# Optimization experiments

Hardware: AMD Instinct MI355X
Metric: run time of the kernel (lower is better)

Reference implementation:

```python
import jax, jax.numpy as jnp
import numpy as np

B, N_TOK, D = 32, 1024, 1024
CH, PS, NP = 3, 16, 32  # channels, patch_size, n_patches (sample_size // patch_size)
EPS = 1e-5


def setup_inputs() -> dict:
    key = jax.random.key(0)
    k1, k2 = jax.random.split(key)
    x = jax.random.normal(k1, (B, N_TOK, D), dtype=jnp.float32)
    ln_w = jnp.ones((D,), dtype=jnp.float32)
    ln_b = jnp.zeros((D,), dtype=jnp.float32)
    W = jax.random.normal(k2, (CH * PS * PS, D), dtype=jnp.float32) * (1.0 / np.sqrt(D))
    b = jnp.zeros((CH * PS * PS,), dtype=jnp.float32)
    return {"x": x, "ln_w": ln_w, "ln_b": ln_b, "W": W, "b": b}


def reference(x, ln_w, ln_b, W, b):
    # LayerNorm over last dim
    mean = jnp.mean(x, axis=-1, keepdims=True)
    var = jnp.mean(jnp.square(x - mean), axis=-1, keepdims=True)
    h = (x - mean) * jax.lax.rsqrt(var + EPS) * ln_w + ln_b
    # SiLU
    h = h * jax.nn.sigmoid(h)
    # Linear: [B, N, D] @ [D, ph*pw*c] + bias
    y = jnp.einsum('bnd,od->bno', h, W) + b  # [B, N_TOK, PS*PS*CH]
    # rearrange 'b (h w) (ph pw c) -> b c (h ph) (w pw)'
    y = y.reshape(B, NP, NP, PS, PS, CH)           # b h w ph pw c
    y = y.transpose(0, 5, 1, 3, 2, 4)              # b c h ph w pw
    y = y.reshape(B, CH, NP * PS, NP * PS)
    return y
```

## Files before the change

kernel.cpp:

```cpp
#include <hip/hip_runtime.h>
#include <hip/hip_bf16.h>

#define M_TOT 32768
#define DDIM  1024
#define ODIM  768
#define LN_EPS 1e-5f

typedef __attribute__((__ext_vector_type__(8))) short bf16x8;
typedef __attribute__((__ext_vector_type__(4))) float f32x4;

__device__ __forceinline__ unsigned short f2bf(float f) {
  union { __hip_bfloat16 h; unsigned short u; } cv;
  cv.h = __float2bfloat16(f);
  return cv.u;
}

__device__ __forceinline__ float silu_f(float v) {
  return v / (1.f + __expf(-v));
}

__global__ void wconv_kernel(const float4* __restrict__ Wf, ushort4* __restrict__ Wb, int n4) {
  int i = blockIdx.x * blockDim.x + threadIdx.x;
  if (i >= n4) return;
  float4 v = Wf[i];
  ushort4 o;
  o.x = f2bf(v.x); o.y = f2bf(v.y); o.z = f2bf(v.z); o.w = f2bf(v.w);
  Wb[i] = o;
}

__global__ __launch_bounds__(256)
void ln_silu_kernel(const float* __restrict__ x, const float* __restrict__ lnw,
                    const float* __restrict__ lnb, __hip_bfloat16* __restrict__ h)
{
  const int tid  = threadIdx.x;
  const int lane = tid & 63;
  const int wid  = tid >> 6;
  const int row  = blockIdx.x * 4 + wid;

  const float4* xr = (const float4*)(x + (size_t)row * DDIM);
  float4 v[4];
#pragma unroll
  for (int jj = 0; jj < 4; ++jj) v[jj] = xr[lane + 64 * jj];

  float s = 0.f, ss = 0.f;
#pragma unroll
  for (int jj = 0; jj < 4; ++jj) {
    float4 a = v[jj];
    s  += a.x + a.y + a.z + a.w;
    ss += a.x * a.x + a.y * a.y + a.z * a.z + a.w * a.w;
  }
#pragma unroll
  for (int off = 1; off < 64; off <<= 1) {
    s  += __shfl_xor(s, off);
    ss += __shfl_xor(ss, off);
  }
  const float mean = s * (1.f / 1024.f);
  const float rstd = rsqrtf(ss * (1.f / 1024.f) - mean * mean + LN_EPS);

  ushort4* hr = (ushort4*)(h + (size_t)row * DDIM);
#pragma unroll
  for (int jj = 0; jj < 4; ++jj) {
    float4 wv = ((const float4*)lnw)[lane + 64 * jj];
    float4 bv = ((const float4*)lnb)[lane + 64 * jj];
    float4 a  = v[jj];
    float e0 = silu_f((a.x - mean) * rstd * wv.x + bv.x);
    float e1 = silu_f((a.y - mean) * rstd * wv.y + bv.y);
    float e2 = silu_f((a.z - mean) * rstd * wv.z + bv.z);
    float e3 = silu_f((a.w - mean) * rstd * wv.w + bv.w);
    ushort4 o; o.x = f2bf(e0); o.y = f2bf(e1); o.z = f2bf(e2); o.w = f2bf(e3);
    hr[lane + 64 * jj] = o;
  }
}

#define GBM 256
#define GBN 192
#define ABYTES 16384
#define BUFB   28672

__device__ __forceinline__ void gload16(const void* g, void* l) {
  __builtin_amdgcn_global_load_lds(
      (const __attribute__((address_space(1))) unsigned int*)g,
      (__attribute__((address_space(3))) unsigned int*)l, 16, 0, 0);
}

#define VMW(n) asm volatile("s_waitcnt vmcnt(" #n ")" ::: "memory")

__global__ __launch_bounds__(512, 2)
void gemm_kernel(const __hip_bfloat16* __restrict__ h,
                 const __hip_bfloat16* __restrict__ Wb,
                 const float* __restrict__ bias,
                 float* __restrict__ out)
{
  __shared__ char smem[4 * BUFB];
  const int tid  = threadIdx.x;
  const int lane = tid & 63;
  const int w    = tid >> 6;

  const int wg = blockIdx.x;
  const int sv = ((wg & 7) << 6) + (wg >> 3);
  const int mt = sv >> 2, nt = sv & 3;
  const int m0 = mt << 8, n0 = nt * GBN;

  const __hip_bfloat16* aP[2]; int aD[2];
#pragma unroll
  for (int q = 0; q < 2; ++q) {
    int s = (q << 9) + tid;
    int row = s >> 2, chk = s & 3;
    aP[q] = h + (size_t)(m0 + row) * DDIM + ((chk ^ ((row >> 1) & 3)) << 3);
    aD[q] = s << 4;
  }
  const bool roleB = (tid < 256);
  const __hip_bfloat16* bP0; int bD0;
  const __hip_bfloat16* bP1; int bD1;
  {
    int s = tid, row = s >> 2, chk = s & 3;
    bP0 = Wb + (size_t)(n0 + row) * DDIM + ((chk ^ ((row >> 1) & 3)) << 3);
    bD0 = ABYTES + (s << 4);
    int s2 = 512 + (tid & 255);
    int r2 = s2 >> 2, c2 = s2 & 3;
    bP1 = Wb + (size_t)(n0 + r2) * DDIM + ((c2 ^ ((r2 >> 1) & 3)) << 3);
    bD1 = ABYTES + (s2 << 4);
  }

  const int wm = w >> 1, wn = w & 1;
  const int lr = lane & 15, lq = lane >> 4;
  int aRd[4], bRd[6];
#pragma unroll
  for (int i = 0; i < 4; ++i) {
    int row = wm * 64 + i * 16 + lr;
    aRd[i] = row * 64 + ((lq ^ ((row >> 1) & 3)) << 4);
  }
#pragma unroll
  for (int j = 0; j < 6; ++j) {
    int row = wn * 96 + j * 16 + lr;
    bRd[j] = ABYTES + row * 64 + ((lq ^ ((row >> 1) & 3)) << 4);
  }

  auto stageA = [&](int t) {
    char* b = smem + (t & 3) * BUFB;
    const int k0 = t << 5;
    gload16(aP[0] + k0, b + aD[0]);
    gload16(aP[1] + k0, b + aD[1]);
  };
  auto stageB = [&](int t) {
    char* b = smem + (t & 3) * BUFB;
    const int k0 = t << 5;
    gload16(bP0 + k0, b + bD0);
    if (roleB) gload16(bP1 + k0, b + bD1);
  };

  f32x4 acc[4][6];
#pragma unroll
  for (int i = 0; i < 4; ++i)
#pragma unroll
    for (int j = 0; j < 6; ++j)
      acc[i][j] = (f32x4){0.f, 0.f, 0.f, 0.f};

  stageA(0); stageB(0);
  stageA(1); stageB(1);
  stageA(2); stageB(2);

  for (int t = 0; t < 32; ++t) {
    if (t <= 29)      { if (roleB) VMW(8); else VMW(6); }
    else if (t == 30) { if (roleB) VMW(4); else VMW(3); }
    else              { VMW(0); }
    __builtin_amdgcn_s_barrier();
    asm volatile("" ::: "memory");

    const char* bb = smem + (t & 3) * BUFB;
    bf16x8 af[4], bf0[3], bf1[3];
#pragma unroll
    for (int i = 0; i < 4; ++i) af[i]  = *(const bf16x8*)(bb + aRd[i]);
#pragma unroll
    for (int j = 0; j < 3; ++j) bf0[j] = *(const bf16x8*)(bb + bRd[j]);
    if (t < 29) stageA(t + 3);

    __builtin_amdgcn_s_setprio(1);
#pragma unroll
    for (int i = 0; i < 4; ++i)
#pragma unroll
      for (int j = 0; j < 3; ++j)
        acc[i][j] = __builtin_amdgcn_mfma_f32_16x16x32_bf16(af[i], bf0[j], acc[i][j], 0, 0, 0);
    __builtin_amdgcn_s_setprio(0);

#pragma unroll
    for (int j = 0; j < 3; ++j) bf1[j] = *(const bf16x8*)(bb + bRd[3 + j]);
    if (t < 29) stageB(t + 3);

    __builtin_amdgcn_s_setprio(1);
#pragma unroll
    for (int i = 0; i < 4; ++i)
#pragma unroll
      for (int j = 0; j < 3; ++j)
        acc[i][3 + j] = __builtin_amdgcn_mfma_f32_16x16x32_bf16(af[i], bf1[j], acc[i][3 + j], 0, 0, 0);
    __builtin_amdgcn_s_setprio(0);
  }

  const int b   = m0 >> 10;
  const int hl0 = (m0 & 1023) >> 5;
  float bv[6]; int cj[6], pwj[6], prj[6];
#pragma unroll
  for (int j = 0; j < 6; ++j) {
    int o = wn * 96 + j * 16 + lr;
    bv[j]  = bias[n0 + o];
    cj[j]  = o % 3;
    int oq = o / 3;
    pwj[j] = oq & 15;
    prj[j] = oq >> 4;
  }
  float* ldsF = (float*)smem;

#pragma unroll
  for (int g = 0; g < 16; ++g) {
    if (wm == (g >> 2)) {
      const int i_f = g & 3;
#pragma unroll
      for (int j = 0; j < 6; ++j)
#pragma unroll
        for (int r = 0; r < 4; ++r) {
          const int tk = lq * 4 + r;
          ldsF[((cj[j] * 4 + prj[j]) << 8) + (tk << 4) + (pwj[j] ^ (lq << 2))] =
              acc[i_f][j][r] + bv[j];
        }
    }
    __syncthreads();
    const int hh = hl0 + (g >> 1);
#pragma unroll
    for (int u = 0; u < 2; ++u) {
      if (u == 1 && tid >= 256) break;
      const int f   = (u << 9) + tid;
      const int c   = f >> 8;
      const int pr  = (f >> 6) & 3;
      const int tk  = (f >> 2) & 15;
      const int pw0 = (f & 3) << 2;
      const int lqw = tk >> 2;
      float4 v = *(const float4*)(ldsF + (((c * 4 + pr) << 8) + (tk << 4)
                                          + (pw0 ^ (lqw << 2))));
      const size_t idx = (((size_t)(b * 3 + c)) << 18)
                       + (size_t)((hh << 4) + (nt << 2) + pr) * 512
                       + ((g & 1) << 8) + (tk << 4) + pw0;
      *(float4*)(out + idx) = v;
    }
    __syncthreads();
  }
}

#define BM 64
#define BK 32
#define NTHR 1024
#define LDS_BYTES 53760

__global__ __launch_bounds__(NTHR, 4)
void fused_kernel(const float* __restrict__ x,
                  const float* __restrict__ lnw,
                  const float* __restrict__ lnb,
                  const float* __restrict__ Wf,
                  const float* __restrict__ bias,
                  float* __restrict__ out)
{
  extern __shared__ char smem[];
  char* AsBase = smem;
  char* BsBase = smem + 4096;
  float* smean = (float*)(smem + 53248);
  float* srstd = smean + BM;

  const int tid = threadIdx.x;
  const int m0  = blockIdx.x * BM;
  const int bb   = m0 >> 10;
  const int h0   = (m0 & 1023) >> 5;

  {
    const int row = tid >> 4;
    const int sub = tid & 15;
    const float4* xr = (const float4*)(x + (size_t)(m0 + row) * DDIM);
    float s = 0.f, ss = 0.f;
#pragma unroll 4
    for (int j = 0; j < 16; ++j) {
      float4 v = xr[sub + (j << 4)];
      s  += v.x + v.y + v.z + v.w;
      ss += v.x * v.x + v.y * v.y + v.z * v.z + v.w * v.w;
    }
#pragma unroll
    for (int off = 1; off < 16; off <<= 1) {
      s  += __shfl_xor(s, off);
      ss += __shfl_xor(ss, off);
    }
    if (sub == 0) {
      float mean = s * (1.f / 1024.f);
      float var  = ss * (1.f / 1024.f) - mean * mean;
      smean[row] = mean;
      srstd[row] = rsqrtf(var + LN_EPS);
    }
  }
  __syncthreads();

  const int arow  = tid >> 4;
  const int acol2 = tid & 15;
  const int aOff  = (m0 + arow) * DDIM + (acol2 << 1);
  const int aDst  = (arow << 6) + ((((acol2 >> 2) ^ ((arow >> 2) & 3)) << 4)) + ((acol2 & 3) << 2);
  const float aMean = smean[arow];
  const float aRstd = srstd[arow];

  int bOffF[6], bDstF[6];
#pragma unroll
  for (int c = 0; c < 6; ++c) {
    int idx = tid + (c << 10);
    int r = idx >> 3, c4 = idx & 7;
    bOffF[c] = r * DDIM + (c4 << 2);
    bDstF[c] = (r << 6) + ((((c4 >> 1) ^ ((r >> 2) & 3)) << 4)) + ((c4 & 1) << 3);
  }

  const int lane = tid & 63;
  const int wid  = tid >> 6;
  const int lr   = lane & 15;
  const int lq   = lane >> 4;
  const int kswz = (lq ^ ((lr >> 2) & 3)) << 4;
  int aRd[4], bRd[3];
#pragma unroll
  for (int i = 0; i < 4; ++i) aRd[i] = (((i << 4) + lr) << 6) + kswz;
#pragma unroll
  for (int j = 0; j < 3; ++j) bRd[j] = ((wid * 48 + (j << 4) + lr) << 6) + kswz;

  float2 aReg, lwReg, lbReg;
  float4 bRegF[6];

  auto loadTile = [&](int tt) {
    const int k0 = tt * BK;
    aReg  = *(const float2*)(x + aOff + k0);
    lwReg = *(const float2*)(lnw + (acol2 << 1) + k0);
    lbReg = *(const float2*)(lnb + (acol2 << 1) + k0);
#pragma unroll
    for (int c = 0; c < 6; ++c)
      bRegF[c] = *(const float4*)(Wf + bOffF[c] + k0);
  };

  auto storeTile = [&]() {
    float hx = (aReg.x - aMean) * aRstd * lwReg.x + lbReg.x;
    float hy = (aReg.y - aMean) * aRstd * lwReg.y + lbReg.y;
    hx = silu_f(hx); hy = silu_f(hy);
    ushort2 ap; ap.x = f2bf(hx); ap.y = f2bf(hy);
    *(ushort2*)(AsBase + aDst) = ap;
#pragma unroll
    for (int c = 0; c < 6; ++c) {
      float4 wv = bRegF[c];
      ushort4 bp; bp.x = f2bf(wv.x); bp.y = f2bf(wv.y); bp.z = f2bf(wv.z); bp.w = f2bf(wv.w);
      *(ushort4*)(BsBase + bDstF[c]) = bp;
    }
  };

  f32x4 acc[4][3];
#pragma unroll
  for (int i = 0; i < 4; ++i)
#pragma unroll
    for (int j = 0; j < 3; ++j)
      acc[i][j] = (f32x4){0.f, 0.f, 0.f, 0.f};

  loadTile(0);
  storeTile();
  __syncthreads();

  for (int t = 0; t < 32; ++t) {
    if (t < 31) loadTile(t + 1);
    bf16x8 af[4], bfr[3];
#pragma unroll
    for (int i = 0; i < 4; ++i) af[i] = *(const bf16x8*)(AsBase + aRd[i]);
#pragma unroll
    for (int j = 0; j < 3; ++j) bfr[j] = *(const bf16x8*)(BsBase + bRd[j]);
#pragma unroll
    for (int i = 0; i < 4; ++i)
#pragma unroll
      for (int j = 0; j < 3; ++j)
        acc[i][j] = __builtin_amdgcn_mfma_f32_16x16x32_bf16(af[i], bfr[j], acc[i][j], 0, 0, 0);
    __syncthreads();
    if (t < 31) storeTile();
    __syncthreads();
  }

  float* ldsF = (float*)smem;
  float bv[3]; int cv[3], phv[3], pwv[3];
#pragma unroll
  for (int j = 0; j < 3; ++j) {
    const int o = wid * 48 + (j << 4) + lr;
    bv[j]  = bias[o];
    cv[j]  = o % 3;
    const int oq = o / 3;
    pwv[j] = oq & 15;
    phv[j] = oq >> 4;
  }

#pragma unroll
  for (int i = 0; i < 4; ++i) {
#pragma unroll
    for (int j = 0; j < 3; ++j) {
#pragma unroll
      for (int r = 0; r < 4; ++r) {
        const int wl  = (lq << 2) + r;
        const int lin = ((cv[j] * 16 + phv[j]) << 8) + (wl << 4) + pwv[j];
        const int dws = lin ^ (cv[j] << 2) ^ (((lin >> 6) & 1) << 4);
        ldsF[dws] = acc[i][j][r] + bv[j];
      }
    }
    __syncthreads();
    const int hq = h0 + (i >> 1);
    const int w0 = (i & 1) << 4;
#pragma unroll
    for (int q = 0; q < 3; ++q) {
      const int g4  = (q << 10) + tid;
      const int dw  = g4 << 2;
      const int run = dw >> 8;
      const int c   = run >> 4;
      const int ph  = run & 15;
      const int wl  = (dw >> 4) & 15;
      const int pw  = dw & 15;
      const int dws = dw ^ (c << 2) ^ (((dw >> 6) & 1) << 4);
      float4 v = *(const float4*)(ldsF + dws);
      const size_t idx = (((size_t)(bb * 3 + c)) << 18)
                       + ((size_t)((hq << 4) + ph) << 9)
                       + ((w0 + wl) << 4) + pw;
      *(float4*)(out + idx) = v;
    }
    __syncthreads();
  }
}

extern "C" void kernel_launch(void* const* d_in, const int* in_sizes, int n_in,
                              void* d_out, int out_size, void* d_ws, size_t ws_size,
                              hipStream_t stream) {
  const float* x    = (const float*)d_in[0];
  const float* lnw  = (const float*)d_in[1];
  const float* lnb  = (const float*)d_in[2];
  const float* W    = (const float*)d_in[3];
  const float* bias = (const float*)d_in[4];
  float* out = (float*)d_out;

  const size_t wbBytes = (size_t)ODIM * DDIM * sizeof(__hip_bfloat16);
  const size_t hBytes  = (size_t)M_TOT * DDIM * sizeof(__hip_bfloat16);
  __hip_bfloat16* Wb = (__hip_bfloat16*)d_ws;
  __hip_bfloat16* hb = (__hip_bfloat16*)((char*)d_ws + wbBytes);

  if (ws_size >= wbBytes + hBytes) {
    wconv_kernel<<<dim3(768), dim3(256), 0, stream>>>((const float4*)W, (ushort4*)Wb,
                                                      ODIM * DDIM / 4);
    ln_silu_kernel<<<dim3(M_TOT / 4), dim3(256), 0, stream>>>(x, lnw, lnb, hb);
    gemm_kernel<<<dim3((M_TOT / GBM) * (ODIM / GBN)), dim3(512), 0, stream>>>(hb, Wb, bias, out);
  } else {
    fused_kernel<<<dim3(M_TOT / BM), dim3(NTHR), LDS_BYTES, stream>>>(
        x, lnw, lnb, W, bias, out);
  }
}
```

Before: 103.4 us.

## Fuse LayerNorm and SiLU into the GEMM A-tile producer

Drops the separate LN+SiLU kernel and its bf16 intermediate buffer. Each GEMM block first computes per-row mean and rstd for its 256 rows from fp32 x. In the main loop it loads x from registers, applies LN+SiLU, packs to bf16 and writes the swizzled A tile into LDS, pipelined one step ahead. This removes the write and re-read of the intermediate activation, but x is now read in fp32 by all four N-tile blocks plus a stats pre-pass. LDS use rises to about 122KB per block, which may cut occupancy.

```diff
diff --git a/kernel.cpp b/kernel.cpp
--- a/kernel.cpp
+++ b/kernel.cpp
@@ -13,6 +13,10 @@
   union { __hip_bfloat16 h; unsigned short u; } cv;
   cv.h = __float2bfloat16(f);
   return cv.u;
+}
+
+__device__ __forceinline__ int pk2(float a, float b) {
+  return (int)((unsigned)f2bf(a) | ((unsigned)f2bf(b) << 16));
 }
 
 __device__ __forceinline__ float silu_f(float v) {
@@ -28,54 +32,14 @@
   Wb[i] = o;
 }
 
-__global__ __launch_bounds__(256)
-void ln_silu_kernel(const float* __restrict__ x, const float* __restrict__ lnw,
-                    const float* __restrict__ lnb, __hip_bfloat16* __restrict__ h)
-{
-  const int tid  = threadIdx.x;
-  const int lane = tid & 63;
-  const int wid  = tid >> 6;
-  const int row  = blockIdx.x * 4 + wid;
-
-  const float4* xr = (const float4*)(x + (size_t)row * DDIM);
-  float4 v[4];
-#pragma unroll
-  for (int jj = 0; jj < 4; ++jj) v[jj] = xr[lane + 64 * jj];
-
-  float s = 0.f, ss = 0.f;
-#pragma unroll
-  for (int jj = 0; jj < 4; ++jj) {
-    float4 a = v[jj];
-    s  += a.x + a.y + a.z + a.w;
-    ss += a.x * a.x + a.y * a.y + a.z * a.z + a.w * a.w;
-  }
-#pragma unroll
-  for (int off = 1; off < 64; off <<= 1) {
-    s  += __shfl_xor(s, off);
-    ss += __shfl_xor(ss, off);
-  }
-  const float mean = s * (1.f / 1024.f);
-  const float rstd = rsqrtf(ss * (1.f / 1024.f) - mean * mean + LN_EPS);
-
-  ushort4* hr = (ushort4*)(h + (size_t)row * DDIM);
-#pragma unroll
-  for (int jj = 0; jj < 4; ++jj) {
-    float4 wv = ((const float4*)lnw)[lane + 64 * jj];
-    float4 bv = ((const float4*)lnb)[lane + 64 * jj];
-    float4 a  = v[jj];
-    float e0 = silu_f((a.x - mean) * rstd * wv.x + bv.x);
-    float e1 = silu_f((a.y - mean) * rstd * wv.y + bv.y);
-    float e2 = silu_f((a.z - mean) * rstd * wv.z + bv.z);
-    float e3 = silu_f((a.w - mean) * rstd * wv.w + bv.w);
-    ushort4 o; o.x = f2bf(e0); o.y = f2bf(e1); o.z = f2bf(e2); o.w = f2bf(e3);
-    hr[lane + 64 * jj] = o;
-  }
-}
-
 #define GBM 256
 #define GBN 192
 #define ABYTES 16384
 #define BUFB   28672
+#define WL_OFF 114688
+#define BL_OFF 118784
+#define SM_OFF 122880
+#define SR_OFF 123904
 
 __device__ __forceinline__ void gload16(const void* g, void* l) {
   __builtin_amdgcn_global_load_lds(
@@ -86,12 +50,19 @@
 #define VMW(n) asm volatile("s_waitcnt vmcnt(" #n ")" ::: "memory")
 
 __global__ __launch_bounds__(512, 2)
-void gemm_kernel(const __hip_bfloat16* __restrict__ h,
-                 const __hip_bfloat16* __restrict__ Wb,
-                 const float* __restrict__ bias,
-                 float* __restrict__ out)
+void gemm_fused_kernel(const float* __restrict__ x,
+                       const float* __restrict__ lnw,
+                       const float* __restrict__ lnb,
+                       const __hip_bfloat16* __restrict__ Wb,
+                       const float* __restrict__ bias,
+                       float* __restrict__ out)
 {
-  __shared__ char smem[4 * BUFB];
+  __shared__ char smem[124928];
+  float* wLds  = (float*)(smem + WL_OFF);
+  float* bLds  = (float*)(smem + BL_OFF);
+  float* smean = (float*)(smem + SM_OFF);
+  float* srstd = (float*)(smem + SR_OFF);
+
   const int tid  = threadIdx.x;
   const int lane = tid & 63;
   const int w    = tid >> 6;
@@ -101,14 +72,43 @@
   const int mt = sv >> 2, nt = sv & 3;
   const int m0 = mt << 8, n0 = nt * GBN;
 
-  const __hip_bfloat16* aP[2]; int aD[2];
-#pragma unroll
-  for (int q = 0; q < 2; ++q) {
-    int s = (q << 9) + tid;
-    int row = s >> 2, chk = s & 3;
-    aP[q] = h + (size_t)(m0 + row) * DDIM + ((chk ^ ((row >> 1) & 3)) << 3);
-    aD[q] = s << 4;
-  }
+  wLds[tid]       = lnw[tid];
+  wLds[tid + 512] = lnw[tid + 512];
+  bLds[tid]       = lnb[tid];
+  bLds[tid + 512] = lnb[tid + 512];
+  {
+    const int srow = tid >> 1;
+    const float4* xr = (const float4*)(x + (size_t)(m0 + srow) * DDIM) + ((tid & 1) << 7);
+    float s0 = 0.f, s1 = 0.f, q0 = 0.f, q1 = 0.f;
+#pragma unroll 4
+    for (int j = 0; j < 128; j += 2) {
+      float4 a = xr[j], b2 = xr[j + 1];
+      s0 += a.x + a.y + a.z + a.w;
+      q0 += a.x * a.x + a.y * a.y + a.z * a.z + a.w * a.w;
+      s1 += b2.x + b2.y + b2.z + b2.w;
+      q1 += b2.x * b2.x + b2.y * b2.y + b2.z * b2.z + b2.w * b2.w;
+    }
+    float s = s0 + s1, q = q0 + q1;
+    s += __shfl_xor(s, 1);
+    q += __shfl_xor(q, 1);
+    if ((tid & 1) == 0) {
+      float mean = s * (1.f / 1024.f);
+      smean[srow] = mean;
+      srstd[srow] = rsqrtf(q * (1.f / 1024.f) - mean * mean + LN_EPS);
+    }
+  }
+  __syncthreads();
+
+  const int row0 = tid >> 2;
+  const int row1 = row0 + 128;
+  const int gc   = tid & 3;
+  const float mean0 = smean[row0], rstd0 = srstd[row0];
+  const float mean1 = smean[row1], rstd1 = srstd[row1];
+  const float* xr0 = x + (size_t)(m0 + row0) * DDIM + (gc << 3);
+  const float* xr1 = x + (size_t)(m0 + row1) * DDIM + (gc << 3);
+  const int aw0 = ((row0 << 2) + (gc ^ ((row0 >> 1) & 3))) << 4;
+  const int aw1 = ((row1 << 2) + (gc ^ ((row1 >> 1) & 3))) << 4;
+
   const bool roleB = (tid < 256);
   const __hip_bfloat16* bP0; int bD0;
   const __hip_bfloat16* bP1; int bD1;
@@ -136,11 +136,47 @@
     bRd[j] = ABYTES + row * 64 + ((lq ^ ((row >> 1) & 3)) << 4);
   }
 
-  auto stageA = [&](int t) {
-    char* b = smem + (t & 3) * BUFB;
-    const int k0 = t << 5;
-    gload16(aP[0] + k0, b + aD[0]);
-    gload16(aP[1] + k0, b + aD[1]);
+  float4 xa0, xa1, xb0, xb1;
+
+  auto xload = [&](int tt) {
+    const int k0 = tt << 5;
+    xa0 = *(const float4*)(xr0 + k0);
+    xa1 = *(const float4*)(xr0 + k0 + 4);
+    xb0 = *(const float4*)(xr1 + k0);
+    xb1 = *(const float4*)(xr1 + k0 + 4);
+  };
+  auto aconv = [&](int tt) {
+    const float* wp = wLds + (tt << 5) + (gc << 3);
+    const float* bp = bLds + (tt << 5) + (gc << 3);
+    float4 w0 = *(const float4*)wp, w1 = *(const float4*)(wp + 4);
+    float4 c0 = *(const float4*)bp, c1 = *(const float4*)(bp + 4);
+    char* dst = smem + (tt & 3) * BUFB;
+    {
+      float h0 = silu_f((xa0.x - mean0) * rstd0 * w0.x + c0.x);
+      float h1 = silu_f((xa0.y - mean0) * rstd0 * w0.y + c0.y);
+      float h2 = silu_f((xa0.z - mean0) * rstd0 * w0.z + c0.z);
+      float h3 = silu_f((xa0.w - mean0) * rstd0 * w0.w + c0.w);
+      float h4 = silu_f((xa1.x - mean0) * rstd0 * w1.x + c1.x);
+      float h5 = silu_f((xa1.y - mean0) * rstd0 * w1.y + c1.y);
+      float h6 = silu_f((xa1.z - mean0) * rstd0 * w1.z + c1.z);
+      float h7 = silu_f((xa1.w - mean0) * rstd0 * w1.w + c1.w);
+      int4 v; v.x = pk2(h0, h1); v.y = pk2(h2, h3);
+      v.z = pk2(h4, h5); v.w = pk2(h6, h7);
+      *(int4*)(dst + aw0) = v;
+    }
+    {
+      float h0 = silu_f((xb0.x - mean1) * rstd1 * w0.x + c0.x);
+      float h1 = silu_f((xb0.y - mean1) * rstd1 * w0.y + c0.y);
+      float h2 = silu_f((xb0.z - mean1) * rstd1 * w0.z + c0.z);
+      float h3 = silu_f((xb0.w - mean1) * rstd1 * w0.w + c0.w);
+      float h4 = silu_f((xb1.x - mean1) * rstd1 * w1.x + c1.x);
+      float h5 = silu_f((xb1.y - mean1) * rstd1 * w1.y + c1.y);
+      float h6 = silu_f((xb1.z - mean1) * rstd1 * w1.z + c1.z);
+      float h7 = silu_f((xb1.w - mean1) * rstd1 * w1.w + c1.w);
+      int4 v; v.x = pk2(h0, h1); v.y = pk2(h2, h3);
+      v.z = pk2(h4, h5); v.w = pk2(h6, h7);
+      *(int4*)(dst + aw1) = v;
+    }
   };
   auto stageB = [&](int t) {
     char* b = smem + (t & 3) * BUFB;
@@ -156,13 +192,16 @@
     for (int j = 0; j < 6; ++j)
       acc[i][j] = (f32x4){0.f, 0.f, 0.f, 0.f};
 
-  stageA(0); stageB(0);
-  stageA(1); stageB(1);
-  stageA(2); stageB(2);
+  xload(0);
+  VMW(0);
+  aconv(0);
+  xload(1);
+  stageB(0); stageB(1); stageB(2);
+  asm volatile("s_waitcnt lgkmcnt(0)" ::: "memory");
 
   for (int t = 0; t < 32; ++t) {
-    if (t <= 29)      { if (roleB) VMW(8); else VMW(6); }
-    else if (t == 30) { if (roleB) VMW(4); else VMW(3); }
+    if (t == 0)       { if (roleB) VMW(4); else VMW(2); }
+    else if (t <= 29) { if (roleB) VMW(2); else VMW(1); }
     else              { VMW(0); }
     __builtin_amdgcn_s_barrier();
     asm volatile("" ::: "memory");
@@ -173,7 +212,10 @@
     for (int i = 0; i < 4; ++i) af[i]  = *(const bf16x8*)(bb + aRd[i]);
 #pragma unroll
     for (int j = 0; j < 3; ++j) bf0[j] = *(const bf16x8*)(bb + bRd[j]);
-    if (t < 29) stageA(t + 3);
+
+    if (t <= 30) aconv(t + 1);
+    if (t <= 29) xload(t + 2);
+    if (t <= 28) stageB(t + 3);
 
     __builtin_amdgcn_s_setprio(1);
 #pragma unroll
@@ -185,7 +227,6 @@
 
 #pragma unroll
     for (int j = 0; j < 3; ++j) bf1[j] = *(const bf16x8*)(bb + bRd[3 + j]);
-    if (t < 29) stageB(t + 3);
 
     __builtin_amdgcn_s_setprio(1);
 #pragma unroll
@@ -194,6 +235,8 @@
       for (int j = 0; j < 3; ++j)
         acc[i][3 + j] = __builtin_amdgcn_mfma_f32_16x16x32_bf16(af[i], bf1[j], acc[i][3 + j], 0, 0, 0);
     __builtin_amdgcn_s_setprio(0);
+
+    asm volatile("s_waitcnt lgkmcnt(0)" ::: "memory");
   }
 
   const int b   = m0 >> 10;
@@ -434,15 +477,13 @@
   float* out = (float*)d_out;
 
   const size_t wbBytes = (size_t)ODIM * DDIM * sizeof(__hip_bfloat16);
-  const size_t hBytes  = (size_t)M_TOT * DDIM * sizeof(__hip_bfloat16);
   __hip_bfloat16* Wb = (__hip_bfloat16*)d_ws;
-  __hip_bfloat16* hb = (__hip_bfloat16*)((char*)d_ws + wbBytes);
-
-  if (ws_size >= wbBytes + hBytes) {
+
+  if (ws_size >= wbBytes) {
     wconv_kernel<<<dim3(768), dim3(256), 0, stream>>>((const float4*)W, (ushort4*)Wb,
                                                       ODIM * DDIM / 4);
-    ln_silu_kernel<<<dim3(M_TOT / 4), dim3(256), 0, stream>>>(x, lnw, lnb, hb);
-    gemm_kernel<<<dim3((M_TOT / GBM) * (ODIM / GBN)), dim3(512), 0, stream>>>(hb, Wb, bias, out);
+    gemm_fused_kernel<<<dim3((M_TOT / GBM) * (ODIM / GBN)), dim3(512), 0, stream>>>(
+        x, lnw, lnb, Wb, bias, out);
   } else {
     fused_kernel<<<dim3(M_TOT / BM), dim3(NTHR), LDS_BYTES, stream>>>(
         x, lnw, lnb, W, bias, out);
```

New measurement: 213.8 us. 107% more time.

## Double GEMM K-tile to 64 with two-stage LDS double buffering

Applied to the files above, without the earlier changes.

Each GEMM iteration now covers a K depth of 64 instead of 32, using an 8-chunk XOR swizzle in LDS. The four-deep ring of K=32 buffers becomes a two-buffer scheme with a single stage prefetched ahead. A and B loads are unified into one staging routine. The aim is to halve the number of barriers and loop iterations and give each wave more MFMA work between syncs. The cost is a shallower prefetch: every iteration waits for all outstanding loads (vmcnt 0), so global-load latency may be exposed more often.

```diff
diff --git a/kernel.cpp b/kernel.cpp
--- a/kernel.cpp
+++ b/kernel.cpp
@@ -74,8 +74,9 @@
 
 #define GBM 256
 #define GBN 192
-#define ABYTES 16384
-#define BUFB   28672
+#define GBK 64
+#define ABY  32768
+#define BUFB 57344
 
 __device__ __forceinline__ void gload16(const void* g, void* l) {
   __builtin_amdgcn_global_load_lds(
@@ -91,7 +92,7 @@
                  const float* __restrict__ bias,
                  float* __restrict__ out)
 {
-  __shared__ char smem[4 * BUFB];
+  __shared__ char smem[2 * BUFB];
   const int tid  = threadIdx.x;
   const int lane = tid & 63;
   const int w    = tid >> 6;
@@ -101,52 +102,47 @@
   const int mt = sv >> 2, nt = sv & 3;
   const int m0 = mt << 8, n0 = nt * GBN;
 
-  const __hip_bfloat16* aP[2]; int aD[2];
-#pragma unroll
-  for (int q = 0; q < 2; ++q) {
+  const __hip_bfloat16* aP[4]; int aD[4];
+#pragma unroll
+  for (int q = 0; q < 4; ++q) {
     int s = (q << 9) + tid;
-    int row = s >> 2, chk = s & 3;
-    aP[q] = h + (size_t)(m0 + row) * DDIM + ((chk ^ ((row >> 1) & 3)) << 3);
+    int row = s >> 3, chk = s & 7;
+    aP[q] = h + (size_t)(m0 + row) * DDIM + ((chk ^ (row & 7)) << 3);
     aD[q] = s << 4;
   }
-  const bool roleB = (tid < 256);
-  const __hip_bfloat16* bP0; int bD0;
-  const __hip_bfloat16* bP1; int bD1;
-  {
-    int s = tid, row = s >> 2, chk = s & 3;
-    bP0 = Wb + (size_t)(n0 + row) * DDIM + ((chk ^ ((row >> 1) & 3)) << 3);
-    bD0 = ABYTES + (s << 4);
-    int s2 = 512 + (tid & 255);
-    int r2 = s2 >> 2, c2 = s2 & 3;
-    bP1 = Wb + (size_t)(n0 + r2) * DDIM + ((c2 ^ ((r2 >> 1) & 3)) << 3);
-    bD1 = ABYTES + (s2 << 4);
+  const __hip_bfloat16* bP[3]; int bD[3];
+#pragma unroll
+  for (int q = 0; q < 3; ++q) {
+    int s = (q << 9) + tid;
+    int row = s >> 3, chk = s & 7;
+    bP[q] = Wb + (size_t)(n0 + row) * DDIM + ((chk ^ (row & 7)) << 3);
+    bD[q] = ABY + (s << 4);
   }
 
   const int wm = w >> 1, wn = w & 1;
   const int lr = lane & 15, lq = lane >> 4;
-  int aRd[4], bRd[6];
-#pragma unroll
-  for (int i = 0; i < 4; ++i) {
-    int row = wm * 64 + i * 16 + lr;
-    aRd[i] = row * 64 + ((lq ^ ((row >> 1) & 3)) << 4);
-  }
-#pragma unroll
-  for (int j = 0; j < 6; ++j) {
-    int row = wn * 96 + j * 16 + lr;
-    bRd[j] = ABYTES + row * 64 + ((lq ^ ((row >> 1) & 3)) << 4);
-  }
-
-  auto stageA = [&](int t) {
-    char* b = smem + (t & 3) * BUFB;
-    const int k0 = t << 5;
-    gload16(aP[0] + k0, b + aD[0]);
-    gload16(aP[1] + k0, b + aD[1]);
-  };
-  auto stageB = [&](int t) {
-    char* b = smem + (t & 3) * BUFB;
-    const int k0 = t << 5;
-    gload16(bP0 + k0, b + bD0);
-    if (roleB) gload16(bP1 + k0, b + bD1);
+  int aRd[8], bRd[12];
+#pragma unroll
+  for (int kk = 0; kk < 2; ++kk) {
+#pragma unroll
+    for (int i = 0; i < 4; ++i) {
+      int row = wm * 64 + i * 16 + lr;
+      aRd[kk * 4 + i] = row * 128 + ((((kk << 2) | lq) ^ (row & 7)) << 4);
+    }
+#pragma unroll
+    for (int j = 0; j < 6; ++j) {
+      int row = wn * 96 + j * 16 + lr;
+      bRd[kk * 6 + j] = ABY + row * 128 + ((((kk << 2) | lq) ^ (row & 7)) << 4);
+    }
+  }
+
+  auto stage = [&](int t) {
+    char* b = smem + (t & 1) * BUFB;
+    const int k0 = t << 6;
+#pragma unroll
+    for (int q = 0; q < 4; ++q) gload16(aP[q] + k0, b + aD[q]);
+#pragma unroll
+    for (int q = 0; q < 3; ++q) gload16(bP[q] + k0, b + bD[q]);
   };
 
   f32x4 acc[4][6];
@@ -156,43 +152,37 @@
     for (int j = 0; j < 6; ++j)
       acc[i][j] = (f32x4){0.f, 0.f, 0.f, 0.f};
 
-  stageA(0); stageB(0);
-  stageA(1); stageB(1);
-  stageA(2); stageB(2);
-
-  for (int t = 0; t < 32; ++t) {
-    if (t <= 29)      { if (roleB) VMW(8); else VMW(6); }
-    else if (t == 30) { if (roleB) VMW(4); else VMW(3); }
-    else              { VMW(0); }
+  stage(0);
+
+  for (int t = 0; t < 16; ++t) {
+    VMW(0);
     __builtin_amdgcn_s_barrier();
     asm volatile("" ::: "memory");
 
-    const char* bb = smem + (t & 3) * BUFB;
-    bf16x8 af[4], bf0[3], bf1[3];
+    const char* bb = smem + (t & 1) * BUFB;
+    if (t < 15) stage(t + 1);
+    bf16x8 af[4], bfq[6];
 #pragma unroll
     for (int i = 0; i < 4; ++i) af[i]  = *(const bf16x8*)(bb + aRd[i]);
 #pragma unroll
-    for (int j = 0; j < 3; ++j) bf0[j] = *(const bf16x8*)(bb + bRd[j]);
-    if (t < 29) stageA(t + 3);
-
+    for (int j = 0; j < 6; ++j) bfq[j] = *(const bf16x8*)(bb + bRd[j]);
     __builtin_amdgcn_s_setprio(1);
 #pragma unroll
     for (int i = 0; i < 4; ++i)
 #pragma unroll
-      for (int j = 0; j < 3; ++j)
-        acc[i][j] = __builtin_amdgcn_mfma_f32_16x16x32_bf16(af[i], bf0[j], acc[i][j], 0, 0, 0);
+      for (int j = 0; j < 6; ++j)
+        acc[i][j] = __builtin_amdgcn_mfma_f32_16x16x32_bf16(af[i], bfq[j], acc[i][j], 0, 0, 0);
     __builtin_amdgcn_s_setprio(0);
-
-#pragma unroll
-    for (int j = 0; j < 3; ++j) bf1[j] = *(const bf16x8*)(bb + bRd[3 + j]);
-    if (t < 29) stageB(t + 3);
-
+#pragma unroll
+    for (int i = 0; i < 4; ++i) af[i]  = *(const bf16x8*)(bb + aRd[4 + i]);
+#pragma unroll
+    for (int j = 0; j < 6; ++j) bfq[j] = *(const bf16x8*)(bb + bRd[6 + j]);
     __builtin_amdgcn_s_setprio(1);
 #pragma unroll
     for (int i = 0; i < 4; ++i)
 #pragma unroll
-      for (int j = 0; j < 3; ++j)
-        acc[i][3 + j] = __builtin_amdgcn_mfma_f32_16x16x32_bf16(af[i], bf1[j], acc[i][3 + j], 0, 0, 0);
+      for (int j = 0; j < 6; ++j)
+        acc[i][j] = __builtin_amdgcn_mfma_f32_16x16x32_bf16(af[i], bfq[j], acc[i][j], 0, 0, 0);
     __builtin_amdgcn_s_setprio(0);
   }
 
```

Result: faster. 100.9 us (-2.4%).
